# Kernel tuning notes

Measured on AMD Instinct MI355X. Metric: run time of the kernel, lower is better.

The kernel has to match this reference:

```python
import jax, jax.numpy as jnp
import numpy as np

B, C, N = 2, 64, 40000
MLP = [64, 64, 128]
EPS = 1e-5


def setup_inputs() -> dict:
    key = jax.random.key(0)
    ks = jax.random.split(key, 2 + 4 * len(MLP))
    inp = {
        "points": jax.random.normal(ks[0], (B, C, N), dtype=jnp.float32),
        "near_idx": jax.random.randint(ks[1], (N, 6), 0, 2 * N, dtype=jnp.int32),
    }
    last = 2 * C
    for i, out_ch in enumerate(MLP):
        k = 2 + 4 * i
        scale = 1.0 / np.sqrt(last)
        inp[f"W{i}"] = jax.random.normal(ks[k], (out_ch, last), dtype=jnp.float32) * scale
        inp[f"b{i}"] = jax.random.normal(ks[k + 1], (out_ch,), dtype=jnp.float32) * 0.01
        inp[f"g{i}"] = jnp.ones((out_ch,), dtype=jnp.float32)
        inp[f"beta{i}"] = jnp.zeros((out_ch,), dtype=jnp.float32)
        last = out_ch
    return inp


def _mlp_bn_relu(x, W, b, g, beta):
    # x: [B, N, 6, Cin]; 1x1 conv == channel matmul
    y = jnp.einsum("bnkc,oc->bnko", x, W) + b
    mu = y.mean(axis=(0, 1, 2))
    var = y.var(axis=(0, 1, 2))  # biased, matches BN training normalization
    y = (y - mu) * jax.lax.rsqrt(var + EPS) * g + beta
    return jax.nn.relu(y)


def reference(points, near_idx, W0, b0, g0, beta0, W1, b1, g1, beta1, W2, b2, g2, beta2):
    x = jnp.transpose(points, (0, 2, 1))          # [B, N, C]
    pad = jnp.full_like(x, -1.0)                  # out-of-index block (-1 fill)
    xpad = jnp.concatenate([x, pad], axis=1)      # [B, 2N, C]
    near = xpad[:, near_idx, :]                   # [B, N, 6, C] irregular gather
    feat = jnp.concatenate(
        [jnp.broadcast_to(x[:, :, None, :], near.shape), near], axis=3
    )                                             # [B, N, 6, 2C]
    feat = _mlp_bn_relu(feat, W0, b0, g0, beta0)
    feat = _mlp_bn_relu(feat, W1, b1, g1, beta1)
    feat = _mlp_bn_relu(feat, W2, b2, g2, beta2)  # [B, N, 6, C']
    new_feature = feat.max(axis=2)                # max over 6 neighbors -> [B, N, C']
    new_feature = jnp.transpose(new_feature, (0, 2, 1))  # [B, C', N] (torch layout)
    out_feature = new_feature.max(axis=1)         # max over channels -> [B, N]
    return (out_feature, new_feature)
```

## Files before the change

kernel.cpp:

```cpp
#include <hip/hip_runtime.h>

typedef unsigned short u16;
typedef unsigned int uint;
typedef short bf16x8 __attribute__((ext_vector_type(8)));
typedef float f32x4 __attribute__((ext_vector_type(4)));

constexpr int B_ = 2;
constexpr int N_ = 40000;
constexpr int SPB = 240000;
constexpr int S_ = B_ * SPB;
constexpr float EPS_ = 1e-5f;
constexpr float INV_S = 1.0f / (float)S_;
constexpr int OF_ = B_ * N_;
constexpr int TILES_PB = SPB / 48;

constexpr int      WS_V_U16   = B_ * N_ * 128;
constexpr size_t   NEED_BIG_B = 81955072ull;

__device__ inline float b2f_lo(uint u) { return __builtin_bit_cast(float, u << 16); }
__device__ inline float b2f_hi(uint u) { return __builtin_bit_cast(float, u & 0xffff0000u); }
__device__ inline u16 f2b(float f) {
    uint b = __builtin_bit_cast(uint, f);
    return (u16)((b + 0x7fffu + ((b >> 16) & 1u)) >> 16);
}
__device__ inline void unp8(uint4 q, float* f) {
    f[0] = b2f_lo(q.x); f[1] = b2f_hi(q.x); f[2] = b2f_lo(q.y); f[3] = b2f_hi(q.y);
    f[4] = b2f_lo(q.z); f[5] = b2f_hi(q.z); f[6] = b2f_lo(q.w); f[7] = b2f_hi(q.w);
}
__device__ inline uint fmap(float f) {
    int i = __float_as_int(f);
    return (i >= 0) ? ((uint)i | 0x80000000u) : ~(uint)i;
}
__device__ inline float funmap(uint u) {
    int i = (u & 0x80000000u) ? (int)(u & 0x7fffffffu) : (int)~u;
    return __int_as_float(i);
}

__global__ __launch_bounds__(256) void wprep_kernel(const float* __restrict__ W0,
                                                    const float* __restrict__ W1,
                                                    const float* __restrict__ W2,
                                                    float* __restrict__ stats,
                                                    float* __restrict__ neg2,
                                                    u16* __restrict__ pack) {
    const int t = threadIdx.x;
    stats[t] = 0.f; stats[t + 256] = 0.f;
    if (t < 64) {
        float s = 0.f;
        for (int j = 0; j < 64; ++j) s += W0[t * 128 + 64 + j];
        neg2[t] = -s;
    }
    for (int g = t; g < 40 * 64; g += 256) {
        int lane = g & 63, grp = g >> 6;
        int cb = lane & 15, kq = lane >> 4;
        ushort4 lo, hi;
        u16* dst;
        if (grp < 16) {
            int ct = grp >> 1, kk = grp & 1;
            int c = ct * 16 + cb, jb = kk * 32 + kq * 8;
            dst = pack + g * 8;
            float v[8];
            #pragma unroll
            for (int i = 0; i < 8; ++i)
                v[i] = (c < 64) ? W0[c * 128 + jb + i] : W0[(c - 64) * 128 + 64 + jb + i];
            lo = {f2b(v[0]), f2b(v[1]), f2b(v[2]), f2b(v[3])};
            hi = {f2b(v[4]), f2b(v[5]), f2b(v[6]), f2b(v[7])};
        } else if (grp < 24) {
            int g2 = grp - 16;
            int ct = g2 >> 1, kk = g2 & 1;
            const float* wp = W1 + (ct * 16 + cb) * 64 + kk * 32 + kq * 8;
            dst = pack + 8192 + (g2 * 64 + lane) * 8;
            lo = {f2b(wp[0]), f2b(wp[1]), f2b(wp[2]), f2b(wp[3])};
            hi = {f2b(wp[4]), f2b(wp[5]), f2b(wp[6]), f2b(wp[7])};
        } else {
            int g3 = grp - 24;
            int ct = g3 >> 1, kk = g3 & 1;
            const float* wp = W2 + (ct * 16 + cb) * 64 + kk * 32 + kq * 8;
            dst = pack + 12288 + (g3 * 64 + lane) * 8;
            lo = {f2b(wp[0]), f2b(wp[1]), f2b(wp[2]), f2b(wp[3])};
            hi = {f2b(wp[4]), f2b(wp[5]), f2b(wp[6]), f2b(wp[7])};
        }
        *(ushort4*)dst = lo;
        *(ushort4*)(dst + 4) = hi;
    }
}

__global__ __launch_bounds__(256) void p0_kernel(const float* __restrict__ pts,
                                                 const u16* __restrict__ pack,
                                                 u16* __restrict__ V) {
    const int t = threadIdx.x, lane = t & 63, w = t >> 6;
    const int cb = lane & 15, kq = lane >> 4;
    const int b = blockIdx.y;
    const int n0 = blockIdx.x * 192 + w * 48;
    const uint4* mp = (const uint4*)pack;

    bf16x8 af[3][2];
    #pragma unroll
    for (int mt = 0; mt < 3; ++mt) {
        int n = n0 + mt * 16 + cb;
        int nc = (n < N_) ? n : (N_ - 1);
        const float* xp = pts + b * 64 * N_ + nc;
        #pragma unroll
        for (int kk = 0; kk < 2; ++kk) {
            int jb = kk * 32 + kq * 8;
            #pragma unroll
            for (int i = 0; i < 8; ++i)
                af[mt][kk][i] = (short)f2b(xp[(size_t)(jb + i) * N_]);
        }
    }
    #pragma unroll
    for (int ct = 0; ct < 8; ++ct) {
        bf16x8 b0 = __builtin_bit_cast(bf16x8, mp[(ct * 2 + 0) * 64 + lane]);
        bf16x8 b1 = __builtin_bit_cast(bf16x8, mp[(ct * 2 + 1) * 64 + lane]);
        #pragma unroll
        for (int mt = 0; mt < 3; ++mt) {
            f32x4 acc = {};
            acc = __builtin_amdgcn_mfma_f32_16x16x32_bf16(af[mt][0], b0, acc, 0, 0, 0);
            acc = __builtin_amdgcn_mfma_f32_16x16x32_bf16(af[mt][1], b1, acc, 0, 0, 0);
            int rbase = n0 + mt * 16 + kq * 4;
            #pragma unroll
            for (int r = 0; r < 4; ++r) {
                int n = rbase + r;
                if (n < N_) V[(size_t)(b * N_ + n) * 128 + ct * 16 + cb] = f2b(acc[r]);
            }
        }
    }
}

__global__ __launch_bounds__(256) void p1_kernel(const u16* __restrict__ V,
                                                 const int* __restrict__ nidx,
                                                 const float* __restrict__ neg2,
                                                 float* __restrict__ stats) {
    const int t = threadIdx.x, lane = t & 63, w = t >> 6;
    const int slot = lane >> 3, cg = lane & 7;
    const int b = blockIdx.y;
    const int s0 = blockIdx.x * 384 + w * 96;
    float ngs8[8];
    #pragma unroll
    for (int i = 0; i < 8; ++i) ngs8[i] = neg2[cg * 8 + i];
    float sum[8] = {0,0,0,0,0,0,0,0}, sq[8] = {0,0,0,0,0,0,0,0};
    #pragma unroll 4
    for (int it = 0; it < 12; ++it) {
        int s = s0 + it * 8 + slot;
        int n = s / 6;
        int m = nidx[s];
        bool valid = (m < N_);
        int row2 = valid ? (b * N_ + m) : 0;
        uint4 q1 = *(const uint4*)(V + (size_t)(b * N_ + n) * 128 + cg * 8);
        uint4 q2 = *(const uint4*)(V + (size_t)row2 * 128 + 64 + cg * 8);
        float v1[8], v2[8];
        unp8(q1, v1); unp8(q2, v2);
        #pragma unroll
        for (int i = 0; i < 8; ++i) {
            float z = v1[i] + (valid ? v2[i] : ngs8[i]);
            sum[i] += z; sq[i] = fmaf(z, z, sq[i]);
        }
    }
    #pragma unroll
    for (int i = 0; i < 8; ++i) {
        sum[i] += __shfl_xor(sum[i], 8); sum[i] += __shfl_xor(sum[i], 16); sum[i] += __shfl_xor(sum[i], 32);
        sq[i]  += __shfl_xor(sq[i], 8);  sq[i]  += __shfl_xor(sq[i], 16);  sq[i]  += __shfl_xor(sq[i], 32);
    }
    __shared__ float red[2][4][64];
    if (slot == 0) {
        #pragma unroll
        for (int i = 0; i < 8; ++i) { red[0][w][cg * 8 + i] = sum[i]; red[1][w][cg * 8 + i] = sq[i]; }
    }
    __syncthreads();
    if (t < 64) {
        float s_ = (red[0][0][t] + red[0][1][t]) + (red[0][2][t] + red[0][3][t]);
        float q_ = (red[1][0][t] + red[1][1][t]) + (red[1][2][t] + red[1][3][t]);
        atomicAdd(&stats[t], s_);
        atomicAdd(&stats[64 + t], q_);
    }
}

__device__ inline bf16x8 build_af(const u16* __restrict__ V, int row1, int row2,
                                  const float* adt0, const float* adt1,
                                  const float* ngs, int j0) {
    float v1f[8], v2f[8];
    uint4 q1 = *(const uint4*)(V + (size_t)row1 * 128 + j0);
    unp8(q1, v1f);
    if (row2 >= 0) {
        uint4 q2 = *(const uint4*)(V + (size_t)row2 * 128 + 64 + j0);
        unp8(q2, v2f);
    } else {
        #pragma unroll
        for (int i = 0; i < 8; ++i) v2f[i] = ngs[j0 + i];
    }
    bf16x8 r;
    #pragma unroll
    for (int i = 0; i < 8; ++i) {
        float f0 = fmaxf((v1f[i] + v2f[i]) * adt0[j0 + i] + adt1[j0 + i], 0.f);
        r[i] = (short)f2b(f0);
    }
    return r;
}

template<int STOREF0>
__global__ __launch_bounds__(256) void p2_kernel(const u16* __restrict__ V,
                                                 const int* __restrict__ nidx,
                                                 const float* __restrict__ neg2,
                                                 const u16* __restrict__ pack,
                                                 const float* __restrict__ g0,
                                                 const float* __restrict__ beta0,
                                                 float* __restrict__ stats,
                                                 u16* __restrict__ f0buf) {
    __shared__ float adt0[64], adt1[64], ngs[64];
    __shared__ float red[2][4][64];
    const int t = threadIdx.x, lane = t & 63, w = t >> 6;
    const int cb = lane & 15, kq = lane >> 4;
    if (t < 64) {
        float mu = stats[t] * INV_S, vr = stats[64 + t] * INV_S - mu * mu;
        float a = rsqrtf(vr + EPS_) * g0[t];
        adt0[t] = a; adt1[t] = beta0[t] - mu * a; ngs[t] = neg2[t];
    }
    __syncthreads();
    const int b = blockIdx.y;
    const int slb = blockIdx.x * 192 + w * 48;
    const uint4* w1p = (const uint4*)(pack + 8192);
    uint4* ftile = STOREF0 ? ((uint4*)f0buf + ((size_t)b * TILES_PB + blockIdx.x * 4 + w) * (6 * 64)) : nullptr;

    bf16x8 bf[4][2];
    #pragma unroll
    for (int ct = 0; ct < 4; ++ct)
        #pragma unroll
        for (int kk = 0; kk < 2; ++kk)
            bf[ct][kk] = __builtin_bit_cast(bf16x8, w1p[(ct * 2 + kk) * 64 + lane]);

    f32x4 acc[3][4] = {};
    #pragma unroll
    for (int mt = 0; mt < 3; ++mt) {
        int sl = slb + mt * 16 + cb;
        int n = sl / 6;
        int m = nidx[sl];
        int row1 = b * N_ + n;
        int row2 = (m < N_) ? (b * N_ + m) : -1;
        bf16x8 af[2];
        #pragma unroll
        for (int kk = 0; kk < 2; ++kk) {
            af[kk] = build_af(V, row1, row2, adt0, adt1, ngs, kk * 32 + kq * 8);
            if constexpr (STOREF0)
                ftile[(mt * 2 + kk) * 64 + lane] = __builtin_bit_cast(uint4, af[kk]);
        }
        #pragma unroll
        for (int ct = 0; ct < 4; ++ct) {
            acc[mt][ct] = __builtin_amdgcn_mfma_f32_16x16x32_bf16(af[0], bf[ct][0], acc[mt][ct], 0, 0, 0);
            acc[mt][ct] = __builtin_amdgcn_mfma_f32_16x16x32_bf16(af[1], bf[ct][1], acc[mt][ct], 0, 0, 0);
        }
    }
    float ssum[4] = {0,0,0,0}, ssq[4] = {0,0,0,0};
    #pragma unroll
    for (int mt = 0; mt < 3; ++mt)
        #pragma unroll
        for (int ct = 0; ct < 4; ++ct)
            #pragma unroll
            for (int r = 0; r < 4; ++r) {
                float z = acc[mt][ct][r];
                ssum[ct] += z; ssq[ct] += z * z;
            }
    #pragma unroll
    for (int ct = 0; ct < 4; ++ct) {
        ssum[ct] += __shfl_xor(ssum[ct], 16); ssum[ct] += __shfl_xor(ssum[ct], 32);
        ssq[ct]  += __shfl_xor(ssq[ct], 16);  ssq[ct]  += __shfl_xor(ssq[ct], 32);
    }
    if (lane < 16) {
        #pragma unroll
        for (int ct = 0; ct < 4; ++ct) {
            red[0][w][ct * 16 + lane] = ssum[ct];
            red[1][w][ct * 16 + lane] = ssq[ct];
        }
    }
    __syncthreads();
    if (t < 64) {
        float s = (red[0][0][t] + red[0][1][t]) + (red[0][2][t] + red[0][3][t]);
        float q = (red[1][0][t] + red[1][1][t]) + (red[1][2][t] + red[1][3][t]);
        atomicAdd(&stats[128 + t], s);
        atomicAdd(&stats[192 + t], q);
    }
}

template<int LOADF0>
__global__ __launch_bounds__(256) void p3_kernel(const u16* __restrict__ V,
                                                 const int* __restrict__ nidx,
                                                 const float* __restrict__ neg2,
                                                 const u16* __restrict__ pack,
                                                 const float* __restrict__ g0, const float* __restrict__ beta0,
                                                 const float* __restrict__ g1, const float* __restrict__ beta1,
                                                 const float* __restrict__ g2,
                                                 float* __restrict__ stats,
                                                 const u16* __restrict__ f0buf,
                                                 float* __restrict__ out) {
    __shared__ u16  f1s[4][3072];
    __shared__ uint bmax[32][128];
    __shared__ float adt0[64], adt1[64], adt2[64], adt3[64], ngs[64];
    __shared__ float psign[128];
    __shared__ float red[2][4][128];
    const int t = threadIdx.x, lane = t & 63, w = t >> 6;
    const int cb = lane & 15, kq = lane >> 4;
    if (t < 64) {
        if constexpr (!LOADF0) {
            float mu0 = stats[t] * INV_S, vr0 = stats[64 + t] * INV_S - mu0 * mu0;
            float a0 = rsqrtf(vr0 + EPS_) * g0[t];
            adt0[t] = a0; adt1[t] = beta0[t] - mu0 * a0;
            ngs[t] = neg2[t];
        }
        float mu1 = stats[128 + t] * INV_S, vr1 = stats[192 + t] * INV_S - mu1 * mu1;
        float a1 = rsqrtf(vr1 + EPS_) * g1[t];
        adt2[t] = a1; adt3[t] = beta1[t] - mu1 * a1;
    }
    if (t < 128) psign[t] = (g2[t] >= 0.f) ? 1.f : -1.f;
    #pragma unroll
    for (int i = 0; i < 16; ++i) ((uint*)bmax)[t + 256 * i] = 0u;
    __syncthreads();

    const int b = blockIdx.y;
    const int slb = blockIdx.x * 192 + w * 48;
    const uint4* w1p = (const uint4*)(pack + 8192);
    const uint4* w2p = (const uint4*)(pack + 12288);
    const uint4* ftile = LOADF0 ? ((const uint4*)f0buf + ((size_t)b * TILES_PB + blockIdx.x * 4 + w) * (6 * 64)) : nullptr;

    bf16x8 bf1[4][2];
    #pragma unroll
    for (int ct = 0; ct < 4; ++ct)
        #pragma unroll
        for (int kk = 0; kk < 2; ++kk)
            bf1[ct][kk] = __builtin_bit_cast(bf16x8, w1p[(ct * 2 + kk) * 64 + lane]);
    f32x4 acc1[3][4] = {};
    #pragma unroll
    for (int mt = 0; mt < 3; ++mt) {
        bf16x8 af[2];
        if constexpr (LOADF0) {
            af[0] = __builtin_bit_cast(bf16x8, ftile[(mt * 2 + 0) * 64 + lane]);
            af[1] = __builtin_bit_cast(bf16x8, ftile[(mt * 2 + 1) * 64 + lane]);
        } else {
            int sl = slb + mt * 16 + cb;
            int n = sl / 6;
            int m = nidx[sl];
            int row1 = b * N_ + n;
            int row2 = (m < N_) ? (b * N_ + m) : -1;
            #pragma unroll
            for (int kk = 0; kk < 2; ++kk)
                af[kk] = build_af(V, row1, row2, adt0, adt1, ngs, kk * 32 + kq * 8);
        }
        #pragma unroll
        for (int ct = 0; ct < 4; ++ct) {
            acc1[mt][ct] = __builtin_amdgcn_mfma_f32_16x16x32_bf16(af[0], bf1[ct][0], acc1[mt][ct], 0, 0, 0);
            acc1[mt][ct] = __builtin_amdgcn_mfma_f32_16x16x32_bf16(af[1], bf1[ct][1], acc1[mt][ct], 0, 0, 0);
        }
    }
    u16* fb = f1s[w];
    #pragma unroll
    for (int mt = 0; mt < 3; ++mt)
        #pragma unroll
        for (int ct = 0; ct < 4; ++ct) {
            float a1c = adt2[ct * 16 + cb], d1c = adt3[ct * 16 + cb];
            #pragma unroll
            for (int r = 0; r < 4; ++r) {
                float f1 = fmaxf(acc1[mt][ct][r] * a1c + d1c, 0.f);
                int rl = mt * 16 + kq * 4 + r;
                fb[rl * 64 + ((ct * 16 + cb) ^ ((rl & 7) << 3))] = f2b(f1);
            }
        }
    float ssum[8] = {0,0,0,0,0,0,0,0}, ssq[8] = {0,0,0,0,0,0,0,0};
    #pragma unroll
    for (int half = 0; half < 2; ++half) {
        bf16x8 bf2[4][2];
        #pragma unroll
        for (int ct = 0; ct < 4; ++ct)
            #pragma unroll
            for (int kk = 0; kk < 2; ++kk)
                bf2[ct][kk] = __builtin_bit_cast(bf16x8, w2p[((half * 4 + ct) * 2 + kk) * 64 + lane]);
        f32x4 acc2[3][4] = {};
        #pragma unroll
        for (int mt = 0; mt < 3; ++mt) {
            int rl = mt * 16 + cb;
            bf16x8 af2[2];
            #pragma unroll
            for (int kk = 0; kk < 2; ++kk) {
                int j0 = kk * 32 + kq * 8;
                uint4 q = *(const uint4*)(fb + rl * 64 + (j0 ^ ((rl & 7) << 3)));
                af2[kk] = __builtin_bit_cast(bf16x8, q);
            }
            #pragma unroll
            for (int ct = 0; ct < 4; ++ct) {
                acc2[mt][ct] = __builtin_amdgcn_mfma_f32_16x16x32_bf16(af2[0], bf2[ct][0], acc2[mt][ct], 0, 0, 0);
                acc2[mt][ct] = __builtin_amdgcn_mfma_f32_16x16x32_bf16(af2[1], bf2[ct][1], acc2[mt][ct], 0, 0, 0);
            }
        }
        #pragma unroll
        for (int ct = 0; ct < 4; ++ct) {
            int c2 = half * 64 + ct * 16 + cb;
            float ps = psign[c2];
            #pragma unroll
            for (int mt = 0; mt < 3; ++mt) {
                int base = mt * 16 + kq * 4;
                int nb = 6 - (base % 6); nb = (nb > 4) ? 4 : nb;
                int nl = w * 8 + base / 6;
                float m1 = -3.402823466e+38f, m2 = -3.402823466e+38f;
                #pragma unroll
                for (int r = 0; r < 4; ++r) {
                    float z = acc2[mt][ct][r];
                    ssum[half * 4 + ct] += z;
                    ssq[half * 4 + ct] += z * z;
                    float zz = z * ps;
                    m1 = (r < nb) ? fmaxf(m1, zz) : m1;
                    m2 = (r < nb) ? m2 : fmaxf(m2, zz);
                }
                atomicMax(&bmax[nl][c2], fmap(m1));
                if (nb < 4) atomicMax(&bmax[nl + 1][c2], fmap(m2));
            }
        }
    }
    #pragma unroll
    for (int j = 0; j < 8; ++j) {
        ssum[j] += __shfl_xor(ssum[j], 16); ssum[j] += __shfl_xor(ssum[j], 32);
        ssq[j]  += __shfl_xor(ssq[j], 16);  ssq[j]  += __shfl_xor(ssq[j], 32);
    }
    if (lane < 16) {
        #pragma unroll
        for (int j = 0; j < 8; ++j) {
            int c = (j >> 2) * 64 + (j & 3) * 16 + lane;
            red[0][w][c] = ssum[j];
            red[1][w][c] = ssq[j];
        }
    }
    __syncthreads();
    if (t < 128) {
        float s = (red[0][0][t] + red[0][1][t]) + (red[0][2][t] + red[0][3][t]);
        float q = (red[1][0][t] + red[1][1][t]) + (red[1][2][t] + red[1][3][t]);
        atomicAdd(&stats[256 + t], s);
        atomicAdd(&stats[384 + t], q);
    }
    {
        int c2 = t >> 1, nh = t & 1;
        float ps = psign[c2];
        float* op = out + OF_ + ((size_t)b * 128 + c2) * N_ + blockIdx.x * 32 + nh * 16;
        #pragma unroll
        for (int i4 = 0; i4 < 4; ++i4) {
            float4 v;
            v.x = funmap(bmax[nh * 16 + i4 * 4 + 0][c2]) * ps;
            v.y = funmap(bmax[nh * 16 + i4 * 4 + 1][c2]) * ps;
            v.z = funmap(bmax[nh * 16 + i4 * 4 + 2][c2]) * ps;
            v.w = funmap(bmax[nh * 16 + i4 * 4 + 3][c2]) * ps;
            *(float4*)(op + i4 * 4) = v;
        }
    }
}

__global__ __launch_bounds__(256) void p4_kernel(const float* __restrict__ g2,
                                                 const float* __restrict__ beta2,
                                                 const float* __restrict__ stats,
                                                 float* __restrict__ outbuf) {
    __shared__ float a2s[128], d2s[128];
    const int t = threadIdx.x;
    if (t < 128) {
        float mu = stats[256 + t] * INV_S;
        float vr = stats[384 + t] * INV_S - mu * mu;
        float a = rsqrtf(vr + EPS_) * g2[t];
        a2s[t] = a;
        d2s[t] = beta2[t] - mu * a;
    }
    __syncthreads();
    const int b = blockIdx.y;
    const int n = blockIdx.x * 256 + t;
    if (n >= N_) return;
    float vmax = -3.402823466e+38f;
    #pragma unroll 8
    for (int c2 = 0; c2 < 128; ++c2) {
        size_t idx = OF_ + ((size_t)b * 128 + c2) * N_ + n;
        float v = fmaxf(outbuf[idx] * a2s[c2] + d2s[c2], 0.f);
        outbuf[idx] = v;
        vmax = fmaxf(vmax, v);
    }
    outbuf[b * N_ + n] = vmax;
}

extern "C" void kernel_launch(void* const* d_in, const int* in_sizes, int n_in,
                              void* d_out, int out_size, void* d_ws, size_t ws_size,
                              hipStream_t stream) {
    (void)in_sizes; (void)n_in; (void)out_size;
    const float* pts   = (const float*)d_in[0];
    const int*   nidx  = (const int*)d_in[1];
    const float* W0    = (const float*)d_in[2];
    const float* g0    = (const float*)d_in[4];
    const float* beta0 = (const float*)d_in[5];
    const float* W1    = (const float*)d_in[6];
    const float* g1    = (const float*)d_in[8];
    const float* beta1 = (const float*)d_in[9];
    const float* W2    = (const float*)d_in[10];
    const float* g2    = (const float*)d_in[12];
    const float* beta2 = (const float*)d_in[13];
    const bool big = ws_size >= NEED_BIG_B;
    u16*   V     = (u16*)d_ws;
    u16*   f0b   = big ? ((u16*)d_ws + WS_V_U16) : nullptr;
    float* stats = (float*)d_ws + (big ? 20480000 : 5120000);
    float* neg2  = stats + 512;
    u16*   pack  = (u16*)d_ws + (big ? 40961152 : 10241152);
    float* out   = (float*)d_out;

    hipLaunchKernelGGL(wprep_kernel, dim3(1), dim3(256), 0, stream, W0, W1, W2, stats, neg2, pack);
    hipLaunchKernelGGL(p0_kernel, dim3((N_ + 191) / 192, B_), dim3(256), 0, stream, pts, pack, V);
    hipLaunchKernelGGL(p1_kernel, dim3(SPB / 384, B_), dim3(256), 0, stream, V, nidx, neg2, stats);
    if (big) {
        hipLaunchKernelGGL((p2_kernel<1>), dim3(SPB / 192, B_), dim3(256), 0, stream,
                           V, nidx, neg2, pack, g0, beta0, stats, f0b);
        hipLaunchKernelGGL((p3_kernel<1>), dim3(SPB / 192, B_), dim3(256), 0, stream,
                           V, nidx, neg2, pack, g0, beta0, g1, beta1, g2, stats, f0b, out);
    } else {
        hipLaunchKernelGGL((p2_kernel<0>), dim3(SPB / 192, B_), dim3(256), 0, stream,
                           V, nidx, neg2, pack, g0, beta0, stats, f0b);
        hipLaunchKernelGGL((p3_kernel<0>), dim3(SPB / 192, B_), dim3(256), 0, stream,
                           V, nidx, neg2, pack, g0, beta0, g1, beta1, g2, stats, f0b, out);
    }
    hipLaunchKernelGGL(p4_kernel, dim3((N_ + 255) / 256, B_), dim3(256), 0, stream, g2, beta2, stats, out);
}
```

Measured before the change: 313.2 us.

## Cache layer-1 pre-activations and remap rows so neighbor max stays in registers

p2 now stores the bf16 layer-1 MFMA outputs (z1) instead of the bf16 layer-0 activations, so p3 can skip the layer-1 matmul and only apply BN+ReLU before layer 2. Rows are permuted through sigma_sl so that each lane's accumulator rows map to fixed point pairs. This lets the max over the 6 neighbors be done in registers and written to plain shared memory, replacing the LDS atomicMax with fmap/funmap encoding. p3 is also restructured to process one 16-row tile at a time, which shrinks the LDS staging buffer and lowers register pressure. The cost is that z1 is rounded to bf16 before BN1, and the index math for the row permutation is more intricate.

```diff
diff --git a/kernel.cpp b/kernel.cpp
--- a/kernel.cpp
+++ b/kernel.cpp
@@ -26,14 +26,6 @@
 __device__ inline void unp8(uint4 q, float* f) {
     f[0] = b2f_lo(q.x); f[1] = b2f_hi(q.x); f[2] = b2f_lo(q.y); f[3] = b2f_hi(q.y);
     f[4] = b2f_lo(q.z); f[5] = b2f_hi(q.z); f[6] = b2f_lo(q.w); f[7] = b2f_hi(q.w);
-}
-__device__ inline uint fmap(float f) {
-    int i = __float_as_int(f);
-    return (i >= 0) ? ((uint)i | 0x80000000u) : ~(uint)i;
-}
-__device__ inline float funmap(uint u) {
-    int i = (u & 0x80000000u) ? (int)(u & 0x7fffffffu) : (int)~u;
-    return __int_as_float(i);
 }
 
 __global__ __launch_bounds__(256) void wprep_kernel(const float* __restrict__ W0,
@@ -196,7 +188,14 @@
     return r;
 }
 
-template<int STOREF0>
+__device__ inline int sigma_sl(int mt, int cb) {
+    int r_ = cb & 3, kqr = cb >> 2;
+    int idx = mt * 4 + r_;
+    int po = (idx >= 6) ? 1 : 0;
+    return (kqr * 2 + po) * 6 + (idx - 6 * po);
+}
+
+template<int STOREZ1>
 __global__ __launch_bounds__(256) void p2_kernel(const u16* __restrict__ V,
                                                  const int* __restrict__ nidx,
                                                  const float* __restrict__ neg2,
@@ -204,7 +203,7 @@
                                                  const float* __restrict__ g0,
                                                  const float* __restrict__ beta0,
                                                  float* __restrict__ stats,
-                                                 u16* __restrict__ f0buf) {
+                                                 u16* __restrict__ z1buf) {
     __shared__ float adt0[64], adt1[64], ngs[64];
     __shared__ float red[2][4][64];
     const int t = threadIdx.x, lane = t & 63, w = t >> 6;
@@ -218,7 +217,7 @@
     const int b = blockIdx.y;
     const int slb = blockIdx.x * 192 + w * 48;
     const uint4* w1p = (const uint4*)(pack + 8192);
-    uint4* ftile = STOREF0 ? ((uint4*)f0buf + ((size_t)b * TILES_PB + blockIdx.x * 4 + w) * (6 * 64)) : nullptr;
+    uint2* ztile = STOREZ1 ? ((uint2*)z1buf + ((size_t)b * TILES_PB + blockIdx.x * 4 + w) * (12 * 64)) : nullptr;
 
     bf16x8 bf[4][2];
     #pragma unroll
@@ -227,37 +226,38 @@
         for (int kk = 0; kk < 2; ++kk)
             bf[ct][kk] = __builtin_bit_cast(bf16x8, w1p[(ct * 2 + kk) * 64 + lane]);
 
-    f32x4 acc[3][4] = {};
+    float ssum[4] = {0,0,0,0}, ssq[4] = {0,0,0,0};
     #pragma unroll
     for (int mt = 0; mt < 3; ++mt) {
-        int sl = slb + mt * 16 + cb;
+        int sl = slb + sigma_sl(mt, cb);
         int n = sl / 6;
         int m = nidx[sl];
         int row1 = b * N_ + n;
         int row2 = (m < N_) ? (b * N_ + m) : -1;
         bf16x8 af[2];
         #pragma unroll
-        for (int kk = 0; kk < 2; ++kk) {
+        for (int kk = 0; kk < 2; ++kk)
             af[kk] = build_af(V, row1, row2, adt0, adt1, ngs, kk * 32 + kq * 8);
-            if constexpr (STOREF0)
-                ftile[(mt * 2 + kk) * 64 + lane] = __builtin_bit_cast(uint4, af[kk]);
-        }
+        f32x4 acc[4] = {};
         #pragma unroll
         for (int ct = 0; ct < 4; ++ct) {
-            acc[mt][ct] = __builtin_amdgcn_mfma_f32_16x16x32_bf16(af[0], bf[ct][0], acc[mt][ct], 0, 0, 0);
-            acc[mt][ct] = __builtin_amdgcn_mfma_f32_16x16x32_bf16(af[1], bf[ct][1], acc[mt][ct], 0, 0, 0);
-        }
-    }
-    float ssum[4] = {0,0,0,0}, ssq[4] = {0,0,0,0};
-    #pragma unroll
-    for (int mt = 0; mt < 3; ++mt)
-        #pragma unroll
-        for (int ct = 0; ct < 4; ++ct)
+            acc[ct] = __builtin_amdgcn_mfma_f32_16x16x32_bf16(af[0], bf[ct][0], acc[ct], 0, 0, 0);
+            acc[ct] = __builtin_amdgcn_mfma_f32_16x16x32_bf16(af[1], bf[ct][1], acc[ct], 0, 0, 0);
+        }
+        #pragma unroll
+        for (int ct = 0; ct < 4; ++ct) {
             #pragma unroll
             for (int r = 0; r < 4; ++r) {
-                float z = acc[mt][ct][r];
-                ssum[ct] += z; ssq[ct] += z * z;
-            }
+                float z = acc[ct][r];
+                ssum[ct] += z; ssq[ct] = fmaf(z, z, ssq[ct]);
+            }
+            if constexpr (STOREZ1) {
+                uint lo = (uint)f2b(acc[ct][0]) | ((uint)f2b(acc[ct][1]) << 16);
+                uint hi = (uint)f2b(acc[ct][2]) | ((uint)f2b(acc[ct][3]) << 16);
+                ztile[(mt * 4 + ct) * 64 + lane] = {lo, hi};
+            }
+        }
+    }
     #pragma unroll
     for (int ct = 0; ct < 4; ++ct) {
         ssum[ct] += __shfl_xor(ssum[ct], 16); ssum[ct] += __shfl_xor(ssum[ct], 32);
@@ -279,7 +279,7 @@
     }
 }
 
-template<int LOADF0>
+template<int LOADZ1>
 __global__ __launch_bounds__(256) void p3_kernel(const u16* __restrict__ V,
                                                  const int* __restrict__ nidx,
                                                  const float* __restrict__ neg2,
@@ -288,129 +288,132 @@
                                                  const float* __restrict__ g1, const float* __restrict__ beta1,
                                                  const float* __restrict__ g2,
                                                  float* __restrict__ stats,
-                                                 const u16* __restrict__ f0buf,
+                                                 const u16* __restrict__ z1buf,
                                                  float* __restrict__ out) {
-    __shared__ u16  f1s[4][3072];
-    __shared__ uint bmax[32][128];
-    __shared__ float adt0[64], adt1[64], adt2[64], adt3[64], ngs[64];
-    __shared__ float psign[128];
+    __shared__ u16   f1t[4][16 * 64];
+    __shared__ float smax[32][129];
     __shared__ float red[2][4][128];
+    __shared__ float adt2s[64], adt3s[64], psign[128];
+    __shared__ float adt0s[64], adt1s[64], ngs[64];
     const int t = threadIdx.x, lane = t & 63, w = t >> 6;
     const int cb = lane & 15, kq = lane >> 4;
     if (t < 64) {
-        if constexpr (!LOADF0) {
+        float mu1 = stats[128 + t] * INV_S, vr1 = stats[192 + t] * INV_S - mu1 * mu1;
+        float a1 = rsqrtf(vr1 + EPS_) * g1[t];
+        adt2s[t] = a1; adt3s[t] = beta1[t] - mu1 * a1;
+        if constexpr (!LOADZ1) {
             float mu0 = stats[t] * INV_S, vr0 = stats[64 + t] * INV_S - mu0 * mu0;
             float a0 = rsqrtf(vr0 + EPS_) * g0[t];
-            adt0[t] = a0; adt1[t] = beta0[t] - mu0 * a0;
-            ngs[t] = neg2[t];
-        }
-        float mu1 = stats[128 + t] * INV_S, vr1 = stats[192 + t] * INV_S - mu1 * mu1;
-        float a1 = rsqrtf(vr1 + EPS_) * g1[t];
-        adt2[t] = a1; adt3[t] = beta1[t] - mu1 * a1;
+            adt0s[t] = a0; adt1s[t] = beta0[t] - mu0 * a0; ngs[t] = neg2[t];
+        }
     }
     if (t < 128) psign[t] = (g2[t] >= 0.f) ? 1.f : -1.f;
-    #pragma unroll
-    for (int i = 0; i < 16; ++i) ((uint*)bmax)[t + 256 * i] = 0u;
     __syncthreads();
 
     const int b = blockIdx.y;
     const int slb = blockIdx.x * 192 + w * 48;
     const uint4* w1p = (const uint4*)(pack + 8192);
     const uint4* w2p = (const uint4*)(pack + 12288);
-    const uint4* ftile = LOADF0 ? ((const uint4*)f0buf + ((size_t)b * TILES_PB + blockIdx.x * 4 + w) * (6 * 64)) : nullptr;
-
-    bf16x8 bf1[4][2];
-    #pragma unroll
-    for (int ct = 0; ct < 4; ++ct)
+    const uint2* zt = LOADZ1 ? ((const uint2*)z1buf + ((size_t)b * TILES_PB + blockIdx.x * 4 + w) * (12 * 64)) : nullptr;
+
+    bf16x8 bf2[8][2];
+    #pragma unroll
+    for (int u = 0; u < 8; ++u)
         #pragma unroll
         for (int kk = 0; kk < 2; ++kk)
-            bf1[ct][kk] = __builtin_bit_cast(bf16x8, w1p[(ct * 2 + kk) * 64 + lane]);
-    f32x4 acc1[3][4] = {};
+            bf2[u][kk] = __builtin_bit_cast(bf16x8, w2p[(u * 2 + kk) * 64 + lane]);
+
+    float a1c[4], d1c[4];
+    #pragma unroll
+    for (int ct = 0; ct < 4; ++ct) { a1c[ct] = adt2s[ct * 16 + cb]; d1c[ct] = adt3s[ct * 16 + cb]; }
+
+    float pmax_[2][4][2];
+    #pragma unroll
+    for (int h = 0; h < 2; ++h)
+        #pragma unroll
+        for (int ct = 0; ct < 4; ++ct) { pmax_[h][ct][0] = -3.402823466e+38f; pmax_[h][ct][1] = -3.402823466e+38f; }
+    float ssum[8] = {0,0,0,0,0,0,0,0}, ssq[8] = {0,0,0,0,0,0,0,0};
+    u16* fb = f1t[w];
+
     #pragma unroll
     for (int mt = 0; mt < 3; ++mt) {
-        bf16x8 af[2];
-        if constexpr (LOADF0) {
-            af[0] = __builtin_bit_cast(bf16x8, ftile[(mt * 2 + 0) * 64 + lane]);
-            af[1] = __builtin_bit_cast(bf16x8, ftile[(mt * 2 + 1) * 64 + lane]);
+        f32x4 z1v[4];
+        if constexpr (LOADZ1) {
+            #pragma unroll
+            for (int ct = 0; ct < 4; ++ct) {
+                uint2 q = zt[(mt * 4 + ct) * 64 + lane];
+                z1v[ct][0] = b2f_lo(q.x); z1v[ct][1] = b2f_hi(q.x);
+                z1v[ct][2] = b2f_lo(q.y); z1v[ct][3] = b2f_hi(q.y);
+            }
         } else {
-            int sl = slb + mt * 16 + cb;
+            bf16x8 bf1[4][2];
+            #pragma unroll
+            for (int ct = 0; ct < 4; ++ct)
+                #pragma unroll
+                for (int kk = 0; kk < 2; ++kk)
+                    bf1[ct][kk] = __builtin_bit_cast(bf16x8, w1p[(ct * 2 + kk) * 64 + lane]);
+            int sl = slb + sigma_sl(mt, cb);
             int n = sl / 6;
             int m = nidx[sl];
             int row1 = b * N_ + n;
             int row2 = (m < N_) ? (b * N_ + m) : -1;
+            bf16x8 af[2];
             #pragma unroll
             for (int kk = 0; kk < 2; ++kk)
-                af[kk] = build_af(V, row1, row2, adt0, adt1, ngs, kk * 32 + kq * 8);
+                af[kk] = build_af(V, row1, row2, adt0s, adt1s, ngs, kk * 32 + kq * 8);
+            #pragma unroll
+            for (int ct = 0; ct < 4; ++ct) {
+                f32x4 a = {};
+                a = __builtin_amdgcn_mfma_f32_16x16x32_bf16(af[0], bf1[ct][0], a, 0, 0, 0);
+                a = __builtin_amdgcn_mfma_f32_16x16x32_bf16(af[1], bf1[ct][1], a, 0, 0, 0);
+                z1v[ct] = a;
+            }
         }
         #pragma unroll
         for (int ct = 0; ct < 4; ++ct) {
-            acc1[mt][ct] = __builtin_amdgcn_mfma_f32_16x16x32_bf16(af[0], bf1[ct][0], acc1[mt][ct], 0, 0, 0);
-            acc1[mt][ct] = __builtin_amdgcn_mfma_f32_16x16x32_bf16(af[1], bf1[ct][1], acc1[mt][ct], 0, 0, 0);
-        }
-    }
-    u16* fb = f1s[w];
-    #pragma unroll
-    for (int mt = 0; mt < 3; ++mt)
-        #pragma unroll
-        for (int ct = 0; ct < 4; ++ct) {
-            float a1c = adt2[ct * 16 + cb], d1c = adt3[ct * 16 + cb];
             #pragma unroll
             for (int r = 0; r < 4; ++r) {
-                float f1 = fmaxf(acc1[mt][ct][r] * a1c + d1c, 0.f);
-                int rl = mt * 16 + kq * 4 + r;
-                fb[rl * 64 + ((ct * 16 + cb) ^ ((rl & 7) << 3))] = f2b(f1);
-            }
-        }
-    float ssum[8] = {0,0,0,0,0,0,0,0}, ssq[8] = {0,0,0,0,0,0,0,0};
-    #pragma unroll
-    for (int half = 0; half < 2; ++half) {
-        bf16x8 bf2[4][2];
-        #pragma unroll
-        for (int ct = 0; ct < 4; ++ct)
-            #pragma unroll
-            for (int kk = 0; kk < 2; ++kk)
-                bf2[ct][kk] = __builtin_bit_cast(bf16x8, w2p[((half * 4 + ct) * 2 + kk) * 64 + lane]);
-        f32x4 acc2[3][4] = {};
-        #pragma unroll
-        for (int mt = 0; mt < 3; ++mt) {
-            int rl = mt * 16 + cb;
-            bf16x8 af2[2];
-            #pragma unroll
-            for (int kk = 0; kk < 2; ++kk) {
-                int j0 = kk * 32 + kq * 8;
-                uint4 q = *(const uint4*)(fb + rl * 64 + (j0 ^ ((rl & 7) << 3)));
-                af2[kk] = __builtin_bit_cast(bf16x8, q);
-            }
+                float f1 = fmaxf(z1v[ct][r] * a1c[ct] + d1c[ct], 0.f);
+                int rw = kq * 4 + r;
+                fb[rw * 64 + ((ct * 16 + cb) ^ ((rw & 7) << 3))] = f2b(f1);
+            }
+        }
+        bf16x8 af2[2];
+        #pragma unroll
+        for (int kk = 0; kk < 2; ++kk) {
+            int j0 = kk * 32 + kq * 8;
+            af2[kk] = __builtin_bit_cast(bf16x8, *(const uint4*)(fb + cb * 64 + (j0 ^ ((cb & 7) << 3))));
+        }
+        #pragma unroll
+        for (int half = 0; half < 2; ++half) {
+            f32x4 acc2[4] = {};
             #pragma unroll
             for (int ct = 0; ct < 4; ++ct) {
-                acc2[mt][ct] = __builtin_amdgcn_mfma_f32_16x16x32_bf16(af2[0], bf2[ct][0], acc2[mt][ct], 0, 0, 0);
-                acc2[mt][ct] = __builtin_amdgcn_mfma_f32_16x16x32_bf16(af2[1], bf2[ct][1], acc2[mt][ct], 0, 0, 0);
-            }
-        }
-        #pragma unroll
-        for (int ct = 0; ct < 4; ++ct) {
-            int c2 = half * 64 + ct * 16 + cb;
-            float ps = psign[c2];
-            #pragma unroll
-            for (int mt = 0; mt < 3; ++mt) {
-                int base = mt * 16 + kq * 4;
-                int nb = 6 - (base % 6); nb = (nb > 4) ? 4 : nb;
-                int nl = w * 8 + base / 6;
-                float m1 = -3.402823466e+38f, m2 = -3.402823466e+38f;
+                acc2[ct] = __builtin_amdgcn_mfma_f32_16x16x32_bf16(af2[0], bf2[half * 4 + ct][0], acc2[ct], 0, 0, 0);
+                acc2[ct] = __builtin_amdgcn_mfma_f32_16x16x32_bf16(af2[1], bf2[half * 4 + ct][1], acc2[ct], 0, 0, 0);
+            }
+            #pragma unroll
+            for (int ct = 0; ct < 4; ++ct) {
+                float ps = psign[half * 64 + ct * 16 + cb];
                 #pragma unroll
                 for (int r = 0; r < 4; ++r) {
-                    float z = acc2[mt][ct][r];
+                    float z = acc2[ct][r];
                     ssum[half * 4 + ct] += z;
-                    ssq[half * 4 + ct] += z * z;
+                    ssq[half * 4 + ct] = fmaf(z, z, ssq[half * 4 + ct]);
                     float zz = z * ps;
-                    m1 = (r < nb) ? fmaxf(m1, zz) : m1;
-                    m2 = (r < nb) ? m2 : fmaxf(m2, zz);
+                    int pi = (mt == 0) ? 0 : ((mt == 2) ? 1 : ((r >= 2) ? 1 : 0));
+                    pmax_[half][ct][pi] = fmaxf(pmax_[half][ct][pi], zz);
                 }
-                atomicMax(&bmax[nl][c2], fmap(m1));
-                if (nb < 4) atomicMax(&bmax[nl + 1][c2], fmap(m2));
-            }
-        }
-    }
+            }
+        }
+    }
+    #pragma unroll
+    for (int half = 0; half < 2; ++half)
+        #pragma unroll
+        for (int ct = 0; ct < 4; ++ct)
+            #pragma unroll
+            for (int p = 0; p < 2; ++p)
+                smax[w * 8 + kq * 2 + p][half * 64 + ct * 16 + cb] = pmax_[half][ct][p];
     #pragma unroll
     for (int j = 0; j < 8; ++j) {
         ssum[j] += __shfl_xor(ssum[j], 16); ssum[j] += __shfl_xor(ssum[j], 32);
@@ -438,10 +441,10 @@
         #pragma unroll
         for (int i4 = 0; i4 < 4; ++i4) {
             float4 v;
-            v.x = funmap(bmax[nh * 16 + i4 * 4 + 0][c2]) * ps;
-            v.y = funmap(bmax[nh * 16 + i4 * 4 + 1][c2]) * ps;
-            v.z = funmap(bmax[nh * 16 + i4 * 4 + 2][c2]) * ps;
-            v.w = funmap(bmax[nh * 16 + i4 * 4 + 3][c2]) * ps;
+            v.x = smax[nh * 16 + i4 * 4 + 0][c2] * ps;
+            v.y = smax[nh * 16 + i4 * 4 + 1][c2] * ps;
+            v.z = smax[nh * 16 + i4 * 4 + 2][c2] * ps;
+            v.w = smax[nh * 16 + i4 * 4 + 3][c2] * ps;
             *(float4*)(op + i4 * 4) = v;
         }
     }
@@ -492,7 +495,7 @@
     const float* beta2 = (const float*)d_in[13];
     const bool big = ws_size >= NEED_BIG_B;
     u16*   V     = (u16*)d_ws;
-    u16*   f0b   = big ? ((u16*)d_ws + WS_V_U16) : nullptr;
+    u16*   z1b   = big ? ((u16*)d_ws + WS_V_U16) : nullptr;
     float* stats = (float*)d_ws + (big ? 20480000 : 5120000);
     float* neg2  = stats + 512;
     u16*   pack  = (u16*)d_ws + (big ? 40961152 : 10241152);
@@ -503,14 +506,14 @@
     hipLaunchKernelGGL(p1_kernel, dim3(SPB / 384, B_), dim3(256), 0, stream, V, nidx, neg2, stats);
     if (big) {
         hipLaunchKernelGGL((p2_kernel<1>), dim3(SPB / 192, B_), dim3(256), 0, stream,
-                           V, nidx, neg2, pack, g0, beta0, stats, f0b);
+                           V, nidx, neg2, pack, g0, beta0, stats, z1b);
         hipLaunchKernelGGL((p3_kernel<1>), dim3(SPB / 192, B_), dim3(256), 0, stream,
-                           V, nidx, neg2, pack, g0, beta0, g1, beta1, g2, stats, f0b, out);
+                           V, nidx, neg2, pack, g0, beta0, g1, beta1, g2, stats, z1b, out);
     } else {
         hipLaunchKernelGGL((p2_kernel<0>), dim3(SPB / 192, B_), dim3(256), 0, stream,
-                           V, nidx, neg2, pack, g0, beta0, stats, f0b);
+                           V, nidx, neg2, pack, g0, beta0, stats, z1b);
         hipLaunchKernelGGL((p3_kernel<0>), dim3(SPB / 192, B_), dim3(256), 0, stream,
-                           V, nidx, neg2, pack, g0, beta0, g1, beta1, g2, stats, f0b, out);
+                           V, nidx, neg2, pack, g0, beta0, g1, beta1, g2, stats, z1b, out);
     }
     hipLaunchKernelGGL(p4_kernel, dim3((N_ + 255) / 256, B_), dim3(256), 0, stream, g2, beta2, stats, out);
 }
```

Measured after the change: 309.1 us. No clear change (-1.3%).
